# Kernel optimization log

Hardware: AMD Instinct MI355X
Metric: run time of the kernel (lower is better)

Reference implementation:

```python
import jax, jax.numpy as jnp
import numpy as np

N = 100_000   # nodes
E = 3_200_000 # directed edges
EC = 16       # edge_channels

def setup_inputs() -> dict:
    key = jax.random.key(0)
    ks = jax.random.split(key, 9)
    x = jax.random.normal(ks[0], (N, 8), jnp.float32)
    adjs = jax.random.randint(ks[1], (2, E), 0, N, jnp.int32)
    edge_attr = jax.random.normal(ks[2], (E, EC), jnp.float32)
    s = 1.0 / np.sqrt(EC)
    lin_e_w = jax.random.uniform(ks[3], (1, EC), jnp.float32, -s, s)
    lin_e_b = jax.random.uniform(ks[4], (1,), jnp.float32, -s, s)
    aggr2_w = jax.random.uniform(ks[5], (1, 4), jnp.float32, -0.5, 0.5)
    aggr2_b = jax.random.uniform(ks[6], (1,), jnp.float32, -0.5, 0.5)
    lin_l_w = jax.random.uniform(ks[7], (1, 1), jnp.float32, -1.0, 1.0)
    lin_l_b = jax.random.uniform(ks[8], (1,), jnp.float32, -1.0, 1.0)
    return dict(x=x, adjs=adjs, edge_attr=edge_attr,
                lin_e_w=lin_e_w, lin_e_b=lin_e_b,
                aggr2_w=aggr2_w, aggr2_b=aggr2_b,
                lin_l_w=lin_l_w, lin_l_b=lin_l_b)

def reference(x, adjs, edge_attr, lin_e_w, lin_e_b, aggr2_w, aggr2_b, lin_l_w, lin_l_b):
    n = x.shape[0]
    # layer 0 (EdgeConv): edge MLP edge_channels -> 1
    ev = (edge_attr @ lin_e_w.T + lin_e_b)[:, 0]            # [E]
    src, dst = adjs[0], adjs[1]
    # to_undirected: edges + reversed edges; row 1 (scatter dest) = cat(dst, src)
    u_idx = jnp.concatenate([dst, src])                      # [2E]
    u_val = jnp.concatenate([ev, ev])                        # [2E]
    cnt = jax.ops.segment_sum(jnp.ones_like(u_val), u_idx, num_segments=n)
    nsum = jax.ops.segment_sum(u_val, u_idx, num_segments=n)
    nmax = jnp.where(cnt > 0, jax.ops.segment_max(u_val, u_idx, num_segments=n), 0.0)
    nmin = jnp.where(cnt > 0, jax.ops.segment_min(u_val, u_idx, num_segments=n), 0.0)
    nmean = nsum / jnp.maximum(cnt, 1.0)                     # torch-scatter mean: 0 for empty

    def inv_clean(node_vals):
        r = 1.0 / node_vals[dst]                             # propagate -> x_i = x[edge_index[1]]
        return jnp.where(jnp.isnan(r) | (r == jnp.inf), 1.0, r)

    nc = jnp.stack([inv_clean(nmax), inv_clean(nmean), inv_clean(nmin), inv_clean(nsum)], axis=1)  # [E,4]
    ec = jnp.where(jnp.isnan(ev) | (ev == jnp.inf), 1.0, ev)[:, None]   # cleaned edge_attr [E,1]
    nc2 = nc @ aggr2_w.T + aggr2_b                            # [E,1]
    out = (ec @ lin_l_w.T + lin_l_b) + nc2 * ec               # [E,1]
    out = jnp.where(out == jnp.inf, 1.0, out)
    return out.reshape(-1)                                    # torch.flatten
```

## Files before the change

### kernel.cpp

```cpp
#include <hip/hip_runtime.h>

#define INF_F (__builtin_inff())
#define PMAX 512
#define G1 1024
#define BT 512
#define NPART 256
#define MARKER 0xFFFFFFFFu


__device__ __forceinline__ unsigned int enc_f(float f) {
    unsigned int u = __float_as_uint(f);
    return (u & 0x80000000u) ? ~u : (u | 0x80000000u);
}
__device__ __forceinline__ float dec_f(unsigned int u) {
    unsigned int b = (u & 0x80000000u) ? (u & 0x7FFFFFFFu) : ~u;
    return __uint_as_float(b);
}
__device__ __forceinline__ float inv_clean(float x) {
    float r = 1.0f / x;
    if (isnan(r) || r == INF_F) r = 1.0f;
    return r;
}
__device__ __forceinline__ float edge_final(float ev, float c, float lw, float lb) {
    float ec = (isnan(ev) || ev == INF_F) ? 1.0f : ev;
    float out = ec * lw + lb + c * ec;
    if (out == INF_F) out = 1.0f;
    return out;
}
__device__ __forceinline__ float dot16_bias(const float* __restrict__ edge_attr,
                                            const float* __restrict__ lin_e_w,
                                            const float* __restrict__ lin_e_b, int e) {
    const float4* ea = reinterpret_cast<const float4*>(edge_attr) + (size_t)e * 4;
    const float4* w4 = reinterpret_cast<const float4*>(lin_e_w);
    float4 a0 = ea[0], a1 = ea[1], a2 = ea[2], a3 = ea[3];
    float4 w0 = w4[0], w1 = w4[1], w2 = w4[2], w3 = w4[3];
    return a0.x * w0.x + a0.y * w0.y + a0.z * w0.z + a0.w * w0.w
         + a1.x * w1.x + a1.y * w1.y + a1.z * w1.z + a1.w * w1.w
         + a2.x * w2.x + a2.y * w2.y + a2.z * w2.z + a2.w * w2.w
         + a3.x * w3.x + a3.y * w3.y + a3.z * w3.z + a3.w * w3.w
         + lin_e_b[0];
}


__global__ void __launch_bounds__(BT)
k1_ev_count(const float* __restrict__ edge_attr,
            const int* __restrict__ src, const int* __restrict__ dst,
            const float* __restrict__ lin_e_w, const float* __restrict__ lin_e_b,
            float* __restrict__ ev_out, unsigned int* __restrict__ gh,
            int E, int P, int CE) {
    __shared__ unsigned int hist[PMAX];
    int t = threadIdx.x, b = blockIdx.x;
    for (int p = t; p < P; p += BT) hist[p] = 0u;
    __syncthreads();
    int start = b * CE, end = min(E, start + CE);
    for (int e = start + t; e < end; e += BT) {
        float ev = dot16_bias(edge_attr, lin_e_w, lin_e_b, e);
        ev_out[e] = ev;
        atomicAdd(&hist[(unsigned int)src[e] >> 8], 1u);
        atomicAdd(&hist[(unsigned int)dst[e] >> 8], 1u);
    }
    __syncthreads();
    for (int p = t; p < P; p += BT) gh[(size_t)b * P + p] = hist[p];
}

__global__ void __launch_bounds__(256)
k2_scan_cols(unsigned int* __restrict__ gh, unsigned int* __restrict__ ptotal, int P) {
    const int VPT = G1 / 256;
    int p = blockIdx.x, t = threadIdx.x;
    unsigned int v[VPT], s = 0u;
    #pragma unroll
    for (int i = 0; i < VPT; ++i) {
        v[i] = (gh[(size_t)(t * VPT + i) * P + p] + 7u) & ~7u;
        s += v[i];
    }
    __shared__ unsigned int sc[256];
    sc[t] = s;
    __syncthreads();
    for (int off = 1; off < 256; off <<= 1) {
        unsigned int x = (t >= off) ? sc[t - off] : 0u;
        __syncthreads();
        sc[t] += x;
        __syncthreads();
    }
    unsigned int run = sc[t] - s;
    #pragma unroll
    for (int i = 0; i < VPT; ++i) {
        gh[(size_t)(t * VPT + i) * P + p] = run;
        run += v[i];
    }
    if (t == 255) ptotal[p] = run;
}

__global__ void k3_scan_part(const unsigned int* __restrict__ ptotal,
                             unsigned int* __restrict__ pbase, int P) {
    int t = threadIdx.x;
    unsigned int u0 = (2 * t < P) ? ptotal[2 * t] : 0u;
    unsigned int u1 = (2 * t + 1 < P) ? ptotal[2 * t + 1] : 0u;
    unsigned int s = u0 + u1;
    __shared__ unsigned int sc[256];
    sc[t] = s;
    __syncthreads();
    for (int off = 1; off < 256; off <<= 1) {
        unsigned int x = (t >= off) ? sc[t - off] : 0u;
        __syncthreads();
        sc[t] += x;
        __syncthreads();
    }
    unsigned int excl = sc[t] - s;
    if (2 * t < P) pbase[2 * t] = excl;
    if (2 * t + 1 < P) pbase[2 * t + 1] = excl + u0;
}

__global__ void __launch_bounds__(BT)
k4_scatter(const int* __restrict__ src, const int* __restrict__ dst,
           const float* __restrict__ ev_in,
           const unsigned int* __restrict__ gh, const unsigned int* __restrict__ pbase,
           const unsigned int* __restrict__ ptotal,
           uint2* __restrict__ rec, int E, int P, int CE) {
    __shared__ unsigned int cur[PMAX];
    int t = threadIdx.x, b = blockIdx.x;
    for (int p = t; p < P; p += BT) cur[p] = pbase[p] + gh[(size_t)b * P + p];
    __syncthreads();
    int start = b * CE, end = min(E, start + CE);
    for (int e = start + t; e < end; e += BT) {
        float ev = ev_in[e];
        unsigned int ebits = __float_as_uint(ev);
        unsigned int s = (unsigned int)src[e], d = (unsigned int)dst[e];
        unsigned int pos = atomicAdd(&cur[d >> 8], 1u);
        rec[pos] = make_uint2(ebits, d & 255u);
        pos = atomicAdd(&cur[s >> 8], 1u);
        rec[pos] = make_uint2(ebits, s & 255u);
    }
    __syncthreads();
    for (int p = t; p < P; p += BT) {
        unsigned int rend = pbase[p] +
            ((b + 1 < G1) ? gh[(size_t)(b + 1) * P + p] : ptotal[p]);
        for (unsigned int q = cur[p]; q < rend; ++q)
            rec[q] = make_uint2(0u, MARKER);
    }
}

__global__ void __launch_bounds__(1024)
k5_reduce(const uint2* __restrict__ rec,
          const unsigned int* __restrict__ pbase, const unsigned int* __restrict__ ptotal,
          const float* __restrict__ aggr2_w, const float* __restrict__ aggr2_b,
          float* __restrict__ nodeC, int N) {
    __shared__ float ssum[NPART];
    __shared__ unsigned int scnt[NPART], smax[NPART], smin[NPART];
    int p = blockIdx.x, t = threadIdx.x;
    if (t < NPART) { ssum[t] = 0.0f; scnt[t] = 0u; smax[t] = 0u; smin[t] = 0xFFFFFFFFu; }
    __syncthreads();
    unsigned int pb = pbase[p], tot = ptotal[p];
    const uint4* r4 = reinterpret_cast<const uint4*>(rec + pb);
    unsigned int n4 = tot >> 1;
    for (unsigned int i = t; i < n4; i += 1024) {
        uint4 q = r4[i];
        if (q.y != MARKER) {
            float v = __uint_as_float(q.x);
            unsigned int eu = enc_f(v);
            atomicAdd(&ssum[q.y], v);
            atomicAdd(&scnt[q.y], 1u);
            atomicMax(&smax[q.y], eu);
            atomicMin(&smin[q.y], eu);
        }
        if (q.w != MARKER) {
            float v = __uint_as_float(q.z);
            unsigned int eu = enc_f(v);
            atomicAdd(&ssum[q.w], v);
            atomicAdd(&scnt[q.w], 1u);
            atomicMax(&smax[q.w], eu);
            atomicMin(&smin[q.w], eu);
        }
    }
    __syncthreads();
    int node = p * NPART + t;
    if (t < NPART && node < N) {
        unsigned int c = scnt[t];
        float sum = ssum[t];
        float mxv = (c > 0u) ? dec_f(smax[t]) : 0.0f;
        float mnv = (c > 0u) ? dec_f(smin[t]) : 0.0f;
        float mean = sum / fmaxf((float)c, 1.0f);
        float4 w = *reinterpret_cast<const float4*>(aggr2_w);
        nodeC[node] = w.x * inv_clean(mxv) + w.y * inv_clean(mean)
                    + w.z * inv_clean(mnv) + w.w * inv_clean(sum) + aggr2_b[0];
    }
}

__global__ void __launch_bounds__(256)
edge_out(float* __restrict__ evout, const int* __restrict__ dst,
         const float* __restrict__ nodeC,
         const float* __restrict__ lin_l_w, const float* __restrict__ lin_l_b,
         int E) {
    int i = blockIdx.x * blockDim.x + threadIdx.x;
    int base = i * 4;
    float lw = lin_l_w[0], lb = lin_l_b[0];
    if (base + 3 < E) {
        float4 ev = *reinterpret_cast<const float4*>(evout + base);
        int4 d = *reinterpret_cast<const int4*>(dst + base);
        float4 o;
        o.x = edge_final(ev.x, nodeC[d.x], lw, lb);
        o.y = edge_final(ev.y, nodeC[d.y], lw, lb);
        o.z = edge_final(ev.z, nodeC[d.z], lw, lb);
        o.w = edge_final(ev.w, nodeC[d.w], lw, lb);
        *reinterpret_cast<float4*>(evout + base) = o;
    } else {
        for (int e = base; e < E; ++e)
            evout[e] = edge_final(evout[e], nodeC[dst[e]], lw, lb);
    }
}


__global__ void init_nodes_fb(unsigned long long* __restrict__ sc,
                              unsigned int* __restrict__ mx,
                              unsigned int* __restrict__ mn, int total) {
    int i = blockIdx.x * blockDim.x + threadIdx.x;
    if (i < total) { sc[i] = 0ull; mx[i] = 0u; mn[i] = 0xFFFFFFFFu; }
}

__global__ void __launch_bounds__(256)
edge_scatter_fb(const float* __restrict__ edge_attr,
                const int* __restrict__ src, const int* __restrict__ dst,
                const float* __restrict__ lin_e_w, const float* __restrict__ lin_e_b,
                float* __restrict__ ev_out,
                unsigned long long* __restrict__ sc,
                unsigned int* __restrict__ mx, unsigned int* __restrict__ mn,
                int E, int N, int repMask) {
    int e = blockIdx.x * blockDim.x + threadIdx.x;
    if (e >= E) return;
    float ev = dot16_bias(edge_attr, lin_e_w, lin_e_b, e);
    ev_out[e] = ev;
    unsigned long long packed =
        (1ull << 52) | (unsigned long long)((ev + 32.0f) * 1048576.0f);
    unsigned int u = enc_f(ev);
    int base = (blockIdx.x & repMask) * N;
    int s = src[e] + base, d = dst[e] + base;
    atomicAdd(&sc[d], packed);
    atomicAdd(&sc[s], packed);
    atomicMax(&mx[d], u);
    atomicMax(&mx[s], u);
    atomicMin(&mn[d], u);
    atomicMin(&mn[s], u);
}

__global__ void node_combine_fb(const unsigned long long* __restrict__ sc,
                                const unsigned int* __restrict__ mx,
                                const unsigned int* __restrict__ mn,
                                const float* __restrict__ aggr2_w,
                                const float* __restrict__ aggr2_b,
                                float* __restrict__ nodeC, int n, int R) {
    int v = blockIdx.x * blockDim.x + threadIdx.x;
    if (v >= n) return;
    unsigned long long acc = 0ull;
    unsigned int M = 0u, m = 0xFFFFFFFFu;
    for (int r = 0; r < R; ++r) {
        acc += sc[(size_t)r * n + v];
        M = max(M, mx[(size_t)r * n + v]);
        m = min(m, mn[(size_t)r * n + v]);
    }
    unsigned long long icnt = acc >> 52;
    float cnt = (float)icnt;
    double sumfix = (double)(acc & ((1ull << 52) - 1ull));
    float sum = (float)(sumfix * (1.0 / 1048576.0) - 32.0 * (double)icnt);
    float mxv, mnv;
    if (icnt > 0) { mxv = dec_f(M); mnv = dec_f(m); }
    else          { mxv = 0.0f;     mnv = 0.0f; }
    float mean = sum / fmaxf(cnt, 1.0f);
    float4 w = *reinterpret_cast<const float4*>(aggr2_w);
    nodeC[v] = w.x * inv_clean(mxv) + w.y * inv_clean(mean)
             + w.z * inv_clean(mnv) + w.w * inv_clean(sum) + aggr2_b[0];
}

static inline size_t align64(size_t x) { return (x + 63) & ~(size_t)63; }

extern "C" void kernel_launch(void* const* d_in, const int* in_sizes, int n_in,
                              void* d_out, int out_size, void* d_ws, size_t ws_size,
                              hipStream_t stream) {
    const int N = in_sizes[0] / 8;
    const int E = in_sizes[1] / 2;

    const int*   adjs      = (const int*)d_in[1];
    const int*   src       = adjs;
    const int*   dst       = adjs + E;
    const float* edge_attr = (const float*)d_in[2];
    const float* lin_e_w   = (const float*)d_in[3];
    const float* lin_e_b   = (const float*)d_in[4];
    const float* aggr2_w   = (const float*)d_in[5];
    const float* aggr2_b   = (const float*)d_in[6];
    const float* lin_l_w   = (const float*)d_in[7];
    const float* lin_l_b   = (const float*)d_in[8];
    float* out = (float*)d_out;

    char* ws = (char*)d_ws;

    const int P = (N + NPART - 1) / NPART;
    const int CE = (E + G1 - 1) / G1;

    size_t max_rec = (size_t)2 * E + (size_t)G1 * P * 8;
    size_t off_gh = 0;
    size_t off_pt = align64(off_gh + (size_t)G1 * P * 4);
    size_t off_pb = align64(off_pt + (size_t)PMAX * 4);
    size_t off_rc = align64(off_pb + (size_t)PMAX * 4);
    size_t off_nc = align64(off_rc + max_rec * 8);
    size_t need_sort = off_nc + (size_t)N * 4;

    if (P <= PMAX && ws_size >= need_sort) {
        unsigned int* gh     = (unsigned int*)(ws + off_gh);
        unsigned int* ptotal = (unsigned int*)(ws + off_pt);
        unsigned int* pbase  = (unsigned int*)(ws + off_pb);
        uint2*        rec    = (uint2*)(ws + off_rc);
        float*        nodeC  = (float*)(ws + off_nc);

        hipLaunchKernelGGL(k1_ev_count, dim3(G1), dim3(BT), 0, stream,
                           edge_attr, src, dst, lin_e_w, lin_e_b, out, gh, E, P, CE);
        hipLaunchKernelGGL(k2_scan_cols, dim3(P), dim3(256), 0, stream, gh, ptotal, P);
        hipLaunchKernelGGL(k3_scan_part, dim3(1), dim3(256), 0, stream, ptotal, pbase, P);
        hipLaunchKernelGGL(k4_scatter, dim3(G1), dim3(BT), 0, stream,
                           src, dst, out, gh, pbase, ptotal, rec, E, P, CE);
        hipLaunchKernelGGL(k5_reduce, dim3(P), dim3(1024), 0, stream,
                           rec, pbase, ptotal, aggr2_w, aggr2_b, nodeC, N);
        int nt = (E + 3) / 4;
        hipLaunchKernelGGL(edge_out, dim3((nt + 255) / 256), dim3(256), 0, stream,
                           out, dst, nodeC, lin_l_w, lin_l_b, E);
    } else {
        int R = 8;
        while (R > 1 && (size_t)R * N * 16 + (size_t)N * 4 > ws_size) R >>= 1;
        unsigned long long* sc    = (unsigned long long*)ws;
        unsigned int*       mx    = (unsigned int*)(sc + (size_t)R * N);
        unsigned int*       mn    = mx + (size_t)R * N;
        float*              nodeC = (float*)(mn + (size_t)R * N);

        int totalRN = R * N;
        hipLaunchKernelGGL(init_nodes_fb, dim3((totalRN + 255) / 256), dim3(256), 0, stream,
                           sc, mx, mn, totalRN);
        hipLaunchKernelGGL(edge_scatter_fb, dim3((E + 255) / 256), dim3(256), 0, stream,
                           edge_attr, src, dst, lin_e_w, lin_e_b,
                           out, sc, mx, mn, E, N, R - 1);
        hipLaunchKernelGGL(node_combine_fb, dim3((N + 255) / 256), dim3(256), 0, stream,
                           sc, mx, mn, aggr2_w, aggr2_b, nodeC, N, R);
        int nt = (E + 3) / 4;
        hipLaunchKernelGGL(edge_out, dim3((nt + 255) / 256), dim3(256), 0, stream,
                           out, dst, nodeC, lin_l_w, lin_l_b, E);
    }
}
```

Before: 173.7 us.

## Fuse bucket-sort pipeline into one cooperative kernel with register-held edges

Replaces the six-kernel counting-sort pipeline with a single cooperative kernel that uses grid.sync between phases: histogram, column scan, partition scan, scatter, per-partition reduce, and the final edge output. Each thread keeps its edges' src, dst and ev values in registers (16 per thread). This avoids re-reading src/dst and ev from global memory and removes the kernel launch gaps. It also removes the old atomic fallback path. In exchange it needs 512 co-resident blocks of 512 threads, adds grid-wide barrier cost, and runs the reduce phase on only about 391 blocks.

```diff
diff --git a/kernel.cpp b/kernel.cpp
--- a/kernel.cpp
+++ b/kernel.cpp
@@ -1,11 +1,19 @@
 #include <hip/hip_runtime.h>
+#include <hip/hip_cooperative_groups.h>
+
+namespace cg = cooperative_groups;
 
 #define INF_F (__builtin_inff())
 #define PMAX 512
+#define NPART 256
+#define MARKER 0xFFFFFFFFu
+
+#define FG 512
+#define FB 512
+#define EPT 16
+
 #define G1 1024
 #define BT 512
-#define NPART 256
-#define MARKER 0xFFFFFFFFu
 
 
 __device__ __forceinline__ unsigned int enc_f(float f) {
@@ -39,6 +47,149 @@
          + a2.x * w2.x + a2.y * w2.y + a2.z * w2.z + a2.w * w2.w
          + a3.x * w3.x + a3.y * w3.y + a3.z * w3.z + a3.w * w3.w
          + lin_e_b[0];
+}
+
+__global__ void __launch_bounds__(FB, 4)
+fused_all(const float* __restrict__ edge_attr,
+          const int* __restrict__ srcA, const int* __restrict__ dstA,
+          const float* __restrict__ lin_e_w, const float* __restrict__ lin_e_b,
+          const float* __restrict__ aggr2_w, const float* __restrict__ aggr2_b,
+          const float* __restrict__ lin_l_w, const float* __restrict__ lin_l_b,
+          unsigned int* __restrict__ gh, unsigned int* __restrict__ ptotal,
+          unsigned int* __restrict__ pbase,
+          uint2* __restrict__ rec, float* __restrict__ nodeC,
+          float* __restrict__ out, int E, int N, int P, int CE) {
+    cg::grid_group grid = cg::this_grid();
+    __shared__ unsigned int shA[PMAX];
+    __shared__ unsigned int shS[FB];
+    __shared__ float ssum[NPART];
+    __shared__ unsigned int scnt[NPART], smax[NPART], smin[NPART];
+
+    const int t = threadIdx.x, b = blockIdx.x;
+    const int start = b * CE, end = min(E, start + CE);
+
+    int   esrc[EPT], edst[EPT];
+    float eev[EPT];
+
+    for (int p = t; p < P; p += FB) shA[p] = 0u;
+    __syncthreads();
+    #pragma unroll
+    for (int i = 0; i < EPT; ++i) {
+        int e = start + i * FB + t;
+        int s = 0, d = 0; float ev = 0.0f;
+        if (e < end) {
+            s = srcA[e]; d = dstA[e];
+            ev = dot16_bias(edge_attr, lin_e_w, lin_e_b, e);
+            atomicAdd(&shA[(unsigned int)s >> 8], 1u);
+            atomicAdd(&shA[(unsigned int)d >> 8], 1u);
+        }
+        esrc[i] = s; edst[i] = d; eev[i] = ev;
+    }
+    __syncthreads();
+    for (int p = t; p < P; p += FB) gh[(size_t)b * P + p] = shA[p];
+    grid.sync();
+
+    if (b < P) {
+        const int p = b;
+        unsigned int v = (gh[(size_t)t * P + p] + 7u) & ~7u;
+        shS[t] = v;
+        __syncthreads();
+        for (int off = 1; off < FB; off <<= 1) {
+            unsigned int x = (t >= off) ? shS[t - off] : 0u;
+            __syncthreads();
+            shS[t] += x;
+            __syncthreads();
+        }
+        unsigned int incl = shS[t];
+        gh[(size_t)t * P + p] = incl - v;
+        if (t == FB - 1) ptotal[p] = incl;
+    }
+    grid.sync();
+
+    if (b == 0) {
+        unsigned int v = (t < P) ? ptotal[t] : 0u;
+        shS[t] = v;
+        __syncthreads();
+        for (int off = 1; off < FB; off <<= 1) {
+            unsigned int x = (t >= off) ? shS[t - off] : 0u;
+            __syncthreads();
+            shS[t] += x;
+            __syncthreads();
+        }
+        if (t < P) pbase[t] = shS[t] - v;
+    }
+    grid.sync();
+
+    for (int p = t; p < P; p += FB) shA[p] = pbase[p] + gh[(size_t)b * P + p];
+    __syncthreads();
+    #pragma unroll
+    for (int i = 0; i < EPT; ++i) {
+        int e = start + i * FB + t;
+        if (e < end) {
+            unsigned int ebits = __float_as_uint(eev[i]);
+            unsigned int s = (unsigned int)esrc[i], d = (unsigned int)edst[i];
+            unsigned int pos = atomicAdd(&shA[d >> 8], 1u);
+            rec[pos] = make_uint2(ebits, d & 255u);
+            pos = atomicAdd(&shA[s >> 8], 1u);
+            rec[pos] = make_uint2(ebits, s & 255u);
+        }
+    }
+    __syncthreads();
+    for (int p = t; p < P; p += FB) {
+        unsigned int rend = pbase[p] +
+            ((b + 1 < FG) ? gh[(size_t)(b + 1) * P + p] : ptotal[p]);
+        for (unsigned int q = shA[p]; q < rend; ++q)
+            rec[q] = make_uint2(0u, MARKER);
+    }
+    grid.sync();
+
+    if (b < P) {
+        if (t < NPART) { ssum[t] = 0.0f; scnt[t] = 0u; smax[t] = 0u; smin[t] = 0xFFFFFFFFu; }
+        __syncthreads();
+        unsigned int pb = pbase[b], tot = ptotal[b];
+        const uint4* r4 = reinterpret_cast<const uint4*>(rec + pb);
+        unsigned int n4 = tot >> 1;
+        for (unsigned int i = t; i < n4; i += FB) {
+            uint4 q = r4[i];
+            if (q.y != MARKER) {
+                float v = __uint_as_float(q.x);
+                unsigned int eu = enc_f(v);
+                atomicAdd(&ssum[q.y], v);
+                atomicAdd(&scnt[q.y], 1u);
+                atomicMax(&smax[q.y], eu);
+                atomicMin(&smin[q.y], eu);
+            }
+            if (q.w != MARKER) {
+                float v = __uint_as_float(q.z);
+                unsigned int eu = enc_f(v);
+                atomicAdd(&ssum[q.w], v);
+                atomicAdd(&scnt[q.w], 1u);
+                atomicMax(&smax[q.w], eu);
+                atomicMin(&smin[q.w], eu);
+            }
+        }
+        __syncthreads();
+        int node = b * NPART + t;
+        if (t < NPART && node < N) {
+            unsigned int c = scnt[t];
+            float sum = ssum[t];
+            float mxv = (c > 0u) ? dec_f(smax[t]) : 0.0f;
+            float mnv = (c > 0u) ? dec_f(smin[t]) : 0.0f;
+            float mean = sum / fmaxf((float)c, 1.0f);
+            float4 w = *reinterpret_cast<const float4*>(aggr2_w);
+            nodeC[node] = w.x * inv_clean(mxv) + w.y * inv_clean(mean)
+                        + w.z * inv_clean(mnv) + w.w * inv_clean(sum) + aggr2_b[0];
+        }
+    }
+    grid.sync();
+
+    float lw = lin_l_w[0], lb = lin_l_b[0];
+    #pragma unroll
+    for (int i = 0; i < EPT; ++i) {
+        int e = start + i * FB + t;
+        if (e < end)
+            out[e] = edge_final(eev[i], nodeC[edst[i]], lw, lb);
+    }
 }
 
 
@@ -209,67 +360,6 @@
     }
 }
 
-
-__global__ void init_nodes_fb(unsigned long long* __restrict__ sc,
-                              unsigned int* __restrict__ mx,
-                              unsigned int* __restrict__ mn, int total) {
-    int i = blockIdx.x * blockDim.x + threadIdx.x;
-    if (i < total) { sc[i] = 0ull; mx[i] = 0u; mn[i] = 0xFFFFFFFFu; }
-}
-
-__global__ void __launch_bounds__(256)
-edge_scatter_fb(const float* __restrict__ edge_attr,
-                const int* __restrict__ src, const int* __restrict__ dst,
-                const float* __restrict__ lin_e_w, const float* __restrict__ lin_e_b,
-                float* __restrict__ ev_out,
-                unsigned long long* __restrict__ sc,
-                unsigned int* __restrict__ mx, unsigned int* __restrict__ mn,
-                int E, int N, int repMask) {
-    int e = blockIdx.x * blockDim.x + threadIdx.x;
-    if (e >= E) return;
-    float ev = dot16_bias(edge_attr, lin_e_w, lin_e_b, e);
-    ev_out[e] = ev;
-    unsigned long long packed =
-        (1ull << 52) | (unsigned long long)((ev + 32.0f) * 1048576.0f);
-    unsigned int u = enc_f(ev);
-    int base = (blockIdx.x & repMask) * N;
-    int s = src[e] + base, d = dst[e] + base;
-    atomicAdd(&sc[d], packed);
-    atomicAdd(&sc[s], packed);
-    atomicMax(&mx[d], u);
-    atomicMax(&mx[s], u);
-    atomicMin(&mn[d], u);
-    atomicMin(&mn[s], u);
-}
-
-__global__ void node_combine_fb(const unsigned long long* __restrict__ sc,
-                                const unsigned int* __restrict__ mx,
-                                const unsigned int* __restrict__ mn,
-                                const float* __restrict__ aggr2_w,
-                                const float* __restrict__ aggr2_b,
-                                float* __restrict__ nodeC, int n, int R) {
-    int v = blockIdx.x * blockDim.x + threadIdx.x;
-    if (v >= n) return;
-    unsigned long long acc = 0ull;
-    unsigned int M = 0u, m = 0xFFFFFFFFu;
-    for (int r = 0; r < R; ++r) {
-        acc += sc[(size_t)r * n + v];
-        M = max(M, mx[(size_t)r * n + v]);
-        m = min(m, mn[(size_t)r * n + v]);
-    }
-    unsigned long long icnt = acc >> 52;
-    float cnt = (float)icnt;
-    double sumfix = (double)(acc & ((1ull << 52) - 1ull));
-    float sum = (float)(sumfix * (1.0 / 1048576.0) - 32.0 * (double)icnt);
-    float mxv, mnv;
-    if (icnt > 0) { mxv = dec_f(M); mnv = dec_f(m); }
-    else          { mxv = 0.0f;     mnv = 0.0f; }
-    float mean = sum / fmaxf(cnt, 1.0f);
-    float4 w = *reinterpret_cast<const float4*>(aggr2_w);
-    nodeC[v] = w.x * inv_clean(mxv) + w.y * inv_clean(mean)
-             + w.z * inv_clean(mnv) + w.w * inv_clean(sum) + aggr2_b[0];
-}
-
 static inline size_t align64(size_t x) { return (x + 63) & ~(size_t)63; }
 
 extern "C" void kernel_launch(void* const* d_in, const int* in_sizes, int n_in,
@@ -291,54 +381,75 @@
     float* out = (float*)d_out;
 
     char* ws = (char*)d_ws;
-
     const int P = (N + NPART - 1) / NPART;
+
+    bool coop_ok = false;
+    {
+        int maxB = 0;
+        hipError_t err = hipOccupancyMaxActiveBlocksPerMultiprocessor(
+            &maxB, reinterpret_cast<const void*>(&fused_all), FB, 0);
+        int numCU = 0;
+        hipError_t err2 = hipDeviceGetAttribute(&numCU,
+            hipDeviceAttributeMultiprocessorCount, 0);
+        if (err == hipSuccess && err2 == hipSuccess &&
+            maxB >= 1 && maxB * numCU >= FG)
+            coop_ok = true;
+    }
+
+    const int CEf = (E + FG - 1) / FG;
+    size_t frec_max = (size_t)2 * E + (size_t)FG * P * 8;
+    size_t f_gh = 0;
+    size_t f_pt = align64(f_gh + (size_t)FG * P * 4);
+    size_t f_pb = align64(f_pt + (size_t)PMAX * 4);
+    size_t f_rc = align64(f_pb + (size_t)PMAX * 4);
+    size_t f_nc = align64(f_rc + frec_max * 8);
+    size_t need_fused = f_nc + (size_t)N * 4;
+
+    if (coop_ok && P <= PMAX && P <= FB && (size_t)E <= (size_t)FG * FB * EPT &&
+        ws_size >= need_fused) {
+        unsigned int* gh     = (unsigned int*)(ws + f_gh);
+        unsigned int* ptotal = (unsigned int*)(ws + f_pt);
+        unsigned int* pbase  = (unsigned int*)(ws + f_pb);
+        uint2*        rec    = (uint2*)(ws + f_rc);
+        float*        nodeC  = (float*)(ws + f_nc);
+
+        void* args[] = {
+            (void*)&edge_attr, (void*)&src, (void*)&dst,
+            (void*)&lin_e_w, (void*)&lin_e_b,
+            (void*)&aggr2_w, (void*)&aggr2_b,
+            (void*)&lin_l_w, (void*)&lin_l_b,
+            (void*)&gh, (void*)&ptotal, (void*)&pbase,
+            (void*)&rec, (void*)&nodeC, (void*)&out,
+            (void*)&E, (void*)&N, (void*)&P, (void*)&CEf
+        };
+        hipLaunchCooperativeKernel(reinterpret_cast<const void*>(&fused_all),
+                                   dim3(FG), dim3(FB), args, 0, stream);
+        return;
+    }
+
     const int CE = (E + G1 - 1) / G1;
-
     size_t max_rec = (size_t)2 * E + (size_t)G1 * P * 8;
     size_t off_gh = 0;
     size_t off_pt = align64(off_gh + (size_t)G1 * P * 4);
     size_t off_pb = align64(off_pt + (size_t)PMAX * 4);
     size_t off_rc = align64(off_pb + (size_t)PMAX * 4);
     size_t off_nc = align64(off_rc + max_rec * 8);
-    size_t need_sort = off_nc + (size_t)N * 4;
-
-    if (P <= PMAX && ws_size >= need_sort) {
-        unsigned int* gh     = (unsigned int*)(ws + off_gh);
-        unsigned int* ptotal = (unsigned int*)(ws + off_pt);
-        unsigned int* pbase  = (unsigned int*)(ws + off_pb);
-        uint2*        rec    = (uint2*)(ws + off_rc);
-        float*        nodeC  = (float*)(ws + off_nc);
-
-        hipLaunchKernelGGL(k1_ev_count, dim3(G1), dim3(BT), 0, stream,
-                           edge_attr, src, dst, lin_e_w, lin_e_b, out, gh, E, P, CE);
-        hipLaunchKernelGGL(k2_scan_cols, dim3(P), dim3(256), 0, stream, gh, ptotal, P);
-        hipLaunchKernelGGL(k3_scan_part, dim3(1), dim3(256), 0, stream, ptotal, pbase, P);
-        hipLaunchKernelGGL(k4_scatter, dim3(G1), dim3(BT), 0, stream,
-                           src, dst, out, gh, pbase, ptotal, rec, E, P, CE);
-        hipLaunchKernelGGL(k5_reduce, dim3(P), dim3(1024), 0, stream,
-                           rec, pbase, ptotal, aggr2_w, aggr2_b, nodeC, N);
-        int nt = (E + 3) / 4;
-        hipLaunchKernelGGL(edge_out, dim3((nt + 255) / 256), dim3(256), 0, stream,
-                           out, dst, nodeC, lin_l_w, lin_l_b, E);
-    } else {
-        int R = 8;
-        while (R > 1 && (size_t)R * N * 16 + (size_t)N * 4 > ws_size) R >>= 1;
-        unsigned long long* sc    = (unsigned long long*)ws;
-        unsigned int*       mx    = (unsigned int*)(sc + (size_t)R * N);
-        unsigned int*       mn    = mx + (size_t)R * N;
-        float*              nodeC = (float*)(mn + (size_t)R * N);
-
-        int totalRN = R * N;
-        hipLaunchKernelGGL(init_nodes_fb, dim3((totalRN + 255) / 256), dim3(256), 0, stream,
-                           sc, mx, mn, totalRN);
-        hipLaunchKernelGGL(edge_scatter_fb, dim3((E + 255) / 256), dim3(256), 0, stream,
-                           edge_attr, src, dst, lin_e_w, lin_e_b,
-                           out, sc, mx, mn, E, N, R - 1);
-        hipLaunchKernelGGL(node_combine_fb, dim3((N + 255) / 256), dim3(256), 0, stream,
-                           sc, mx, mn, aggr2_w, aggr2_b, nodeC, N, R);
-        int nt = (E + 3) / 4;
-        hipLaunchKernelGGL(edge_out, dim3((nt + 255) / 256), dim3(256), 0, stream,
-                           out, dst, nodeC, lin_l_w, lin_l_b, E);
-    }
-}
+
+    unsigned int* gh     = (unsigned int*)(ws + off_gh);
+    unsigned int* ptotal = (unsigned int*)(ws + off_pt);
+    unsigned int* pbase  = (unsigned int*)(ws + off_pb);
+    uint2*        rec    = (uint2*)(ws + off_rc);
+    float*        nodeC  = (float*)(ws + off_nc);
+
+    hipLaunchKernelGGL(k1_ev_count, dim3(G1), dim3(BT), 0, stream,
+                       edge_attr, src, dst, lin_e_w, lin_e_b, out, gh, E, P, CE);
+    hipLaunchKernelGGL(k2_scan_cols, dim3(P), dim3(256), 0, stream, gh, ptotal, P);
+    hipLaunchKernelGGL(k3_scan_part, dim3(1), dim3(256), 0, stream, ptotal, pbase, P);
+    hipLaunchKernelGGL(k4_scatter, dim3(G1), dim3(BT), 0, stream,
+                       src, dst, out, gh, pbase, ptotal, rec, E, P, CE);
+    hipLaunchKernelGGL(k5_reduce, dim3(P), dim3(1024), 0, stream,
+                       rec, pbase, ptotal, aggr2_w, aggr2_b, nodeC, N);
+    int nt = (E + 3) / 4;
+    hipLaunchKernelGGL(edge_out, dim3((nt + 255) / 256), dim3(256), 0, stream,
+                       out, dst, nodeC, lin_l_w, lin_l_b, E);
+}
```

Result: no change. 173.1 us (-0.3%).

## Stage partitioned edge records in LDS before writing contiguous runs to global

Applied to the files above, without the earlier changes.

The scatter kernel now buckets each block's edge records into a shared-memory buffer using a local prefix scan over partition counts, pads the gaps with markers locally, then copies the buffer out so consecutive threads write consecutive global slots within each partition. This replaces random per-record global writes with mostly coalesced runs. It adds a large LDS allocation (limiting occupancy), a per-element binary search, and a fallback condition on LDS capacity.

```diff
diff --git a/kernel.cpp b/kernel.cpp
--- a/kernel.cpp
+++ b/kernel.cpp
@@ -4,8 +4,10 @@
 #define PMAX 512
 #define G1 1024
 #define BT 512
+#define BT4 1024
 #define NPART 256
 #define MARKER 0xFFFFFFFFu
+#define LREC 9856
 
 
 __device__ __forceinline__ unsigned int enc_f(float f) {
@@ -111,32 +113,67 @@
     if (2 * t + 1 < P) pbase[2 * t + 1] = excl + u0;
 }
 
-__global__ void __launch_bounds__(BT)
-k4_scatter(const int* __restrict__ src, const int* __restrict__ dst,
-           const float* __restrict__ ev_in,
-           const unsigned int* __restrict__ gh, const unsigned int* __restrict__ pbase,
-           const unsigned int* __restrict__ ptotal,
-           uint2* __restrict__ rec, int E, int P, int CE) {
-    __shared__ unsigned int cur[PMAX];
-    int t = threadIdx.x, b = blockIdx.x;
-    for (int p = t; p < P; p += BT) cur[p] = pbase[p] + gh[(size_t)b * P + p];
-    __syncthreads();
-    int start = b * CE, end = min(E, start + CE);
-    for (int e = start + t; e < end; e += BT) {
+__global__ void __launch_bounds__(BT4)
+k4_staged(const int* __restrict__ src, const int* __restrict__ dst,
+          const float* __restrict__ ev_in,
+          const unsigned int* __restrict__ gh, const unsigned int* __restrict__ pbase,
+          const unsigned int* __restrict__ ptotal,
+          uint2* __restrict__ rec, int E, int P, int CE) {
+    __shared__ uint2 lrec[LREC];
+    __shared__ unsigned int lstart[PMAX + 1];
+    __shared__ unsigned int lcur[PMAX];
+    __shared__ unsigned int goff[PMAX];
+    __shared__ unsigned int sc[512];
+
+    const int t = threadIdx.x, b = blockIdx.x;
+
+    for (int p = t; p < P; p += BT4) {
+        unsigned int g0 = gh[(size_t)b * P + p];
+        unsigned int g1 = (b + 1 < G1) ? gh[(size_t)(b + 1) * P + p] : ptotal[p];
+        lcur[p] = g1 - g0;
+        goff[p] = pbase[p] + g0;
+    }
+    __syncthreads();
+
+    unsigned int v = (t < P) ? lcur[t] : 0u;
+    if (t < 512) sc[t] = v;
+    __syncthreads();
+    for (int off = 1; off < 512; off <<= 1) {
+        unsigned int x = 0u;
+        if (t < 512 && t >= off) x = sc[t - off];
+        __syncthreads();
+        if (t < 512) sc[t] += x;
+        __syncthreads();
+    }
+    if (t < P) { lstart[t] = sc[t] - v; lcur[t] = sc[t] - v; }
+    if (t == P - 1) lstart[P] = sc[t];
+    __syncthreads();
+
+    const int start = b * CE, end = min(E, start + CE);
+    for (int e = start + t; e < end; e += BT4) {
         float ev = ev_in[e];
         unsigned int ebits = __float_as_uint(ev);
         unsigned int s = (unsigned int)src[e], d = (unsigned int)dst[e];
-        unsigned int pos = atomicAdd(&cur[d >> 8], 1u);
-        rec[pos] = make_uint2(ebits, d & 255u);
-        pos = atomicAdd(&cur[s >> 8], 1u);
-        rec[pos] = make_uint2(ebits, s & 255u);
-    }
-    __syncthreads();
-    for (int p = t; p < P; p += BT) {
-        unsigned int rend = pbase[p] +
-            ((b + 1 < G1) ? gh[(size_t)(b + 1) * P + p] : ptotal[p]);
-        for (unsigned int q = cur[p]; q < rend; ++q)
-            rec[q] = make_uint2(0u, MARKER);
+        unsigned int pos = atomicAdd(&lcur[d >> 8], 1u);
+        lrec[pos] = make_uint2(ebits, d & 255u);
+        pos = atomicAdd(&lcur[s >> 8], 1u);
+        lrec[pos] = make_uint2(ebits, s & 255u);
+    }
+    __syncthreads();
+
+    for (int p = t; p < P; p += BT4)
+        for (unsigned int q = lcur[p]; q < lstart[p + 1]; ++q)
+            lrec[q] = make_uint2(0u, MARKER);
+    __syncthreads();
+
+    const unsigned int tot = lstart[P];
+    for (unsigned int j = t; j < tot; j += BT4) {
+        int lo = 0, hi = P;
+        while (hi - lo > 1) {
+            int mid = (lo + hi) >> 1;
+            if (lstart[mid] <= j) lo = mid; else hi = mid;
+        }
+        rec[goff[lo] + (j - lstart[lo])] = lrec[j];
     }
 }
 
@@ -303,7 +340,9 @@
     size_t off_nc = align64(off_rc + max_rec * 8);
     size_t need_sort = off_nc + (size_t)N * 4;
 
-    if (P <= PMAX && ws_size >= need_sort) {
+    bool lds_ok = ((size_t)2 * CE + (size_t)7 * P) <= LREC;
+
+    if (P <= PMAX && lds_ok && ws_size >= need_sort) {
         unsigned int* gh     = (unsigned int*)(ws + off_gh);
         unsigned int* ptotal = (unsigned int*)(ws + off_pt);
         unsigned int* pbase  = (unsigned int*)(ws + off_pb);
@@ -314,7 +353,7 @@
                            edge_attr, src, dst, lin_e_w, lin_e_b, out, gh, E, P, CE);
         hipLaunchKernelGGL(k2_scan_cols, dim3(P), dim3(256), 0, stream, gh, ptotal, P);
         hipLaunchKernelGGL(k3_scan_part, dim3(1), dim3(256), 0, stream, ptotal, pbase, P);
-        hipLaunchKernelGGL(k4_scatter, dim3(G1), dim3(BT), 0, stream,
+        hipLaunchKernelGGL(k4_staged, dim3(G1), dim3(BT4), 0, stream,
                            src, dst, out, gh, pbase, ptotal, rec, E, P, CE);
         hipLaunchKernelGGL(k5_reduce, dim3(P), dim3(1024), 0, stream,
                            rec, pbase, ptotal, aggr2_w, aggr2_b, nodeC, N);
```

Result: faster. 167.1 us (-3.8%).
